# Kernel tuning notes

Measured on AMD Instinct MI355X. Metric: run time of the kernel, lower is better.

Reference implementation:

```python
import jax, jax.numpy as jnp
import numpy as np

B, T, D = 8, 4096, 256
GATE_MIN, GATE_MAX = 0.01, 0.99


def setup_inputs() -> dict:
    key = jax.random.key(0)
    ks = jax.random.split(key, 8)
    inp = {
        "x_re": jax.random.normal(ks[0], (B, T, D), jnp.float32),
        "x_im": jax.random.normal(ks[1], (B, T, D), jnp.float32),
        "s0_re": jnp.zeros((B, D), jnp.float32),
        "s0_im": jnp.zeros((B, D), jnp.float32),
        "decay_re": jax.random.normal(ks[2], (D,), jnp.float32),
        "decay_im": 0.1 * jax.random.normal(ks[3], (D,), jnp.float32),
        "Wm": 0.02 * jax.random.normal(ks[4], (2 * D, 2 * D), jnp.float32)
              + jnp.eye(2 * D, dtype=jnp.float32),  # eye_ init on diag blocks
        "bm": jnp.zeros((2 * D,), jnp.float32),
        "Wo": 0.02 * jax.random.normal(ks[5], (2 * D, 2 * D), jnp.float32),
        "bo": jnp.zeros((2 * D,), jnp.float32),
        "Wg": 0.02 * jax.random.normal(ks[6], (D, 2 * D), jnp.float32),
        "bg": jnp.zeros((D,), jnp.float32),
    }
    return inp


def reference(x_re, x_im, s0_re, s0_im, decay_re, decay_im,
              Wm, bm, Wo, bo, Wg, bg):
    # decay = sigmoid(decay_re) + i*decay_im
    dr = jax.nn.sigmoid(decay_re)
    di = decay_im

    # scan over time: inputs as [T, B, D]
    xs = (jnp.swapaxes(x_re, 0, 1), jnp.swapaxes(x_im, 0, 1))

    def step(carry, xt):
        s_re, s_im = carry
        xr, xi = xt                                   # [B, D]
        x_cat = jnp.concatenate([xr, xi], axis=-1)    # [B, 2D]
        x_in = x_cat @ Wm.T + bm
        ur, ui = jnp.split(x_in, 2, axis=-1)
        # complex mul-add: new_state = prev_state * decay + update
        ns_re = s_re * dr - s_im * di + ur
        ns_im = s_re * di + s_im * dr + ui
        s_cat = jnp.concatenate([ns_re, ns_im], axis=-1)  # [B, 2D]
        source = s_cat @ Wo.T + bo                        # [B, 2D] (re|im)
        gate = jnp.clip(jax.nn.sigmoid(s_cat @ Wg.T + bg), GATE_MIN, GATE_MAX)
        y = jnp.concatenate([source, gate], axis=-1)      # [B, 3D]
        return (ns_re, ns_im), y

    _, ys = jax.lax.scan(step, (s0_re, s0_im), xs)        # [T, B, 3D]
    return jnp.swapaxes(ys, 0, 1)                          # [B, T, 3D] = [src_re|src_im|gate]
```

## Files before the change

### kernel.cpp

```cpp
#include <hip/hip_runtime.h>
#include <hip/hip_bf16.h>
#include <cstdint>
#include <cstddef>


typedef __bf16 bf16;
typedef __bf16 bf16x4 __attribute__((ext_vector_type(4)));
typedef __bf16 bf16x8 __attribute__((ext_vector_type(8)));
typedef float floatx4 __attribute__((ext_vector_type(4)));

#define NB 8
#define NT 4096
#define ND 256
#define BT (NB * NT)
#define TWOD 512
#define CHUNK 128
#define NCHUNK (NT / CHUNK)

static __device__ __forceinline__ float sigmoidf_(float x) {
  return 1.0f / (1.0f + __expf(-x));
}

static __device__ __forceinline__ void async_copy16(const void* g, void* l) {
  __builtin_amdgcn_global_load_lds(
      (__attribute__((address_space(1))) void*)g,
      (__attribute__((address_space(3))) void*)l, 16, 0, 0);
}

__global__ void k_prep(const float* __restrict__ xr,
                       const float* __restrict__ xi,
                       const float* __restrict__ Wm,
                       const float* __restrict__ Wo,
                       const float* __restrict__ Wg,
                       const float* __restrict__ bo,
                       const float* __restrict__ bg,
                       bf16* __restrict__ X,
                       bf16* __restrict__ Wm_b,
                       bf16* __restrict__ Wc_b,
                       float* __restrict__ bc) {
  const int bid = blockIdx.x;
  if (bid < 8192) {
    const int idx = (bid * 256 + threadIdx.x) * 4;
    const int row = idx >> 8;
    const int dd = idx & 255;
    const float4 vr = *(const float4*)(xr + idx);
    const float4 vi = *(const float4*)(xi + idx);
    bf16x4 br, bi;
    br[0] = (bf16)vr.x; br[1] = (bf16)vr.y; br[2] = (bf16)vr.z; br[3] = (bf16)vr.w;
    bi[0] = (bf16)vi.x; bi[1] = (bf16)vi.y; bi[2] = (bf16)vi.z; bi[3] = (bf16)vi.w;
    *(bf16x4*)(X + (size_t)row * TWOD + dd) = br;
    *(bf16x4*)(X + (size_t)row * TWOD + ND + dd) = bi;
  } else {
    const int i = (bid - 8192) * 256 + threadIdx.x;
    Wm_b[i] = (bf16)Wm[i];
    Wc_b[i] = (bf16)Wo[i];
    if (i < 131072) Wc_b[262144 + i] = (bf16)Wg[i];
    if (i < 512) bc[i] = bo[i];
    if (i < 256) bc[512 + i] = bg[i];
  }
}

template <int MODE>
__global__ __launch_bounds__(256) void gemm_bt(
    const bf16* __restrict__ A, const bf16* __restrict__ Bw,
    const float* __restrict__ bias, void* __restrict__ Cout,
    const int K, const int N, const int actStart) {
  __shared__ __align__(16) bf16 As[128 * 64];
  __shared__ __align__(16) bf16 Bs[128 * 64];
  const int tid = threadIdx.x;
  const int wave = tid >> 6;
  const int lane = tid & 63;
  const int quad = lane >> 4;
  const int l16 = lane & 15;
  const int m0 = blockIdx.x * 128;
  const int n0 = blockIdx.y * 128;
  const int wm = (wave >> 1) * 64;
  const int wn = (wave & 1) * 64;

  const int srow = lane >> 3;
  const int schunk = (lane & 7) ^ (srow & 7);

  floatx4 acc[4][4];
#pragma unroll
  for (int i = 0; i < 4; ++i)
#pragma unroll
    for (int j = 0; j < 4; ++j) acc[i][j] = (floatx4)0.0f;

  for (int k0 = 0; k0 < K; k0 += 64) {
    __syncthreads();
#pragma unroll
    for (int i = 0; i < 4; ++i) {
      const int seg = wave * 4 + i;
      const int row = seg * 8 + srow;
      async_copy16(A + (size_t)(m0 + row) * K + k0 + schunk * 8, As + seg * 512);
      async_copy16(Bw + (size_t)(n0 + row) * K + k0 + schunk * 8, Bs + seg * 512);
    }
    __syncthreads();

#pragma unroll
    for (int s = 0; s < 2; ++s) {
      bf16x8 af[4], bfr[4];
#pragma unroll
      for (int mi = 0; mi < 4; ++mi) {
        const int row = wm + mi * 16 + l16;
        const int ch = ((s << 2) | quad) ^ (l16 & 7);
        af[mi] = *(const bf16x8*)(As + row * 64 + ch * 8);
      }
#pragma unroll
      for (int ni = 0; ni < 4; ++ni) {
        const int row = wn + ni * 16 + l16;
        const int ch = ((s << 2) | quad) ^ (l16 & 7);
        bfr[ni] = *(const bf16x8*)(Bs + row * 64 + ch * 8);
      }
#pragma unroll
      for (int mi = 0; mi < 4; ++mi)
#pragma unroll
        for (int ni = 0; ni < 4; ++ni)
          acc[mi][ni] = __builtin_amdgcn_mfma_f32_16x16x32_bf16(
              af[mi], bfr[ni], acc[mi][ni], 0, 0, 0);
    }
  }

#pragma unroll
  for (int mi = 0; mi < 4; ++mi) {
    const int rb = m0 + wm + mi * 16 + quad * 4;
#pragma unroll
    for (int ni = 0; ni < 4; ++ni) {
      const int col = n0 + wn + ni * 16 + l16;
      const float bb = bias[col];
      if (MODE == 0) {
        bf16* C = (bf16*)Cout;
#pragma unroll
        for (int r = 0; r < 4; ++r)
          C[(size_t)(rb + r) * N + col] = (bf16)(acc[mi][ni][r] + bb);
      } else {
        float* C = (float*)Cout;
#pragma unroll
        for (int r = 0; r < 4; ++r) {
          float v = acc[mi][ni][r] + bb;
          if (col >= actStart) v = fminf(fmaxf(sigmoidf_(v), 0.01f), 0.99f);
          C[(size_t)(rb + r) * N + col] = v;
        }
      }
    }
  }
}

__global__ void k_scan_pass1(const bf16* __restrict__ U,
                             const float* __restrict__ decay_re,
                             const float* __restrict__ decay_im,
                             float* __restrict__ Fre, float* __restrict__ Fim) {
  const int d = threadIdx.x;
  const int c = blockIdx.x;
  const int b = blockIdx.y;
  const float dr = sigmoidf_(decay_re[d]);
  const float di = decay_im[d];
  float sr = 0.f, si = 0.f;
  const size_t rowbase = (size_t)b * NT + (size_t)c * CHUNK;
  const bf16* Ur = U + rowbase * TWOD + d;
#pragma unroll 4
  for (int j = 0; j < CHUNK; ++j) {
    const float ur = (float)Ur[(size_t)j * TWOD];
    const float ui = (float)Ur[(size_t)j * TWOD + ND];
    const float nr = sr * dr - si * di + ur;
    const float ni = sr * di + si * dr + ui;
    sr = nr; si = ni;
  }
  const int o = (b * NCHUNK + c) * ND + d;
  Fre[o] = sr; Fim[o] = si;
}

__global__ void k_scan_pass2(const float* __restrict__ Fre,
                             const float* __restrict__ Fim,
                             const float* __restrict__ s0_re,
                             const float* __restrict__ s0_im,
                             const float* __restrict__ decay_re,
                             const float* __restrict__ decay_im,
                             float* __restrict__ Ire, float* __restrict__ Iim) {
  const int d = threadIdx.x;
  const int b = blockIdx.x;
  const float dr = sigmoidf_(decay_re[d]);
  const float di = decay_im[d];
  float pr = dr, pi = di;
#pragma unroll
  for (int i = 0; i < 7; ++i) {
    const float nr = pr * pr - pi * pi;
    const float ni = 2.f * pr * pi;
    pr = nr; pi = ni;
  }
  float sr = s0_re[b * ND + d];
  float si = s0_im[b * ND + d];
  for (int c = 0; c < NCHUNK; ++c) {
    const int o = (b * NCHUNK + c) * ND + d;
    Ire[o] = sr; Iim[o] = si;
    const float nr = sr * pr - si * pi + Fre[o];
    const float ni = sr * pi + si * pr + Fim[o];
    sr = nr; si = ni;
  }
}

__global__ void k_scan_pass3(bf16* __restrict__ U,
                             const float* __restrict__ decay_re,
                             const float* __restrict__ decay_im,
                             const float* __restrict__ Ire,
                             const float* __restrict__ Iim) {
  const int d = threadIdx.x;
  const int c = blockIdx.x;
  const int b = blockIdx.y;
  const float dr = sigmoidf_(decay_re[d]);
  const float di = decay_im[d];
  const int o = (b * NCHUNK + c) * ND + d;
  float sr = Ire[o], si = Iim[o];
  const size_t rowbase = (size_t)b * NT + (size_t)c * CHUNK;
  bf16* Ur = U + rowbase * TWOD + d;
#pragma unroll 4
  for (int j = 0; j < CHUNK; ++j) {
    const float ur = (float)Ur[(size_t)j * TWOD];
    const float ui = (float)Ur[(size_t)j * TWOD + ND];
    const float nr = sr * dr - si * di + ur;
    const float ni = sr * di + si * dr + ui;
    sr = nr; si = ni;
    Ur[(size_t)j * TWOD] = (bf16)nr;
    Ur[(size_t)j * TWOD + ND] = (bf16)ni;
  }
}


extern "C" void kernel_launch(void* const* d_in, const int* in_sizes, int n_in,
                              void* d_out, int out_size, void* d_ws, size_t ws_size,
                              hipStream_t stream) {
  const float* x_re = (const float*)d_in[0];
  const float* x_im = (const float*)d_in[1];
  const float* s0_re = (const float*)d_in[2];
  const float* s0_im = (const float*)d_in[3];
  const float* decay_re = (const float*)d_in[4];
  const float* decay_im = (const float*)d_in[5];
  const float* Wm = (const float*)d_in[6];
  const float* bm = (const float*)d_in[7];
  const float* Wo = (const float*)d_in[8];
  const float* bo = (const float*)d_in[9];
  const float* Wg = (const float*)d_in[10];
  const float* bg = (const float*)d_in[11];

  char* ws = (char*)d_ws;
  const size_t XCAT_OFF = 0;
  const size_t U_OFF = 33554432;
  const size_t WM_OFF = 67108864;
  const size_t WC_OFF = WM_OFF + 524288;
  const size_t BC_OFF = WC_OFF + 786432;
  const size_t FRE_OFF = BC_OFF + 4096;
  const size_t FIM_OFF = FRE_OFF + 262144;
  const size_t IRE_OFF = FIM_OFF + 262144;
  const size_t IIM_OFF = IRE_OFF + 262144;

  bf16* Xcat = (bf16*)(ws + XCAT_OFF);
  bf16* U = (bf16*)(ws + U_OFF);
  bf16* Wm_b = (bf16*)(ws + WM_OFF);
  bf16* Wc_b = (bf16*)(ws + WC_OFF);
  float* bc = (float*)(ws + BC_OFF);
  float* Fre = (float*)(ws + FRE_OFF);
  float* Fim = (float*)(ws + FIM_OFF);
  float* Ire = (float*)(ws + IRE_OFF);
  float* Iim = (float*)(ws + IIM_OFF);

  k_prep<<<dim3(9216), 256, 0, stream>>>(x_re, x_im, Wm, Wo, Wg, bo, bg,
                                         Xcat, Wm_b, Wc_b, bc);
  gemm_bt<0><<<dim3(256, 4), 256, 0, stream>>>(Xcat, Wm_b, bm, U, 512, 512, 0);
  k_scan_pass1<<<dim3(NCHUNK, NB), ND, 0, stream>>>(U, decay_re, decay_im, Fre, Fim);
  k_scan_pass2<<<dim3(NB), ND, 0, stream>>>(Fre, Fim, s0_re, s0_im, decay_re, decay_im, Ire, Iim);
  k_scan_pass3<<<dim3(NCHUNK, NB), ND, 0, stream>>>(U, decay_re, decay_im, Ire, Iim);
  gemm_bt<1><<<dim3(256, 6), 256, 0, stream>>>(U, Wc_b, bc, d_out, 512, 768, 512);
}
```

Measured before the change: 266.5 us.

## Fuse input bf16 conversion into GEMM, interleave re/im columns, shrink scan chunks

After: 259.8 us. -2.5%, faster.

```diff
diff --git a/kernel.cpp b/kernel.cpp
--- a/kernel.cpp
+++ b/kernel.cpp
@@ -5,7 +5,6 @@
 
 
 typedef __bf16 bf16;
-typedef __bf16 bf16x4 __attribute__((ext_vector_type(4)));
 typedef __bf16 bf16x8 __attribute__((ext_vector_type(8)));
 typedef float floatx4 __attribute__((ext_vector_type(4)));
 
@@ -14,7 +13,7 @@
 #define ND 256
 #define BT (NB * NT)
 #define TWOD 512
-#define CHUNK 128
+#define CHUNK 32
 #define NCHUNK (NT / CHUNK)
 
 static __device__ __forceinline__ float sigmoidf_(float x) {
@@ -27,44 +26,38 @@
       (__attribute__((address_space(3))) void*)l, 16, 0, 0);
 }
 
-__global__ void k_prep(const float* __restrict__ xr,
-                       const float* __restrict__ xi,
-                       const float* __restrict__ Wm,
+union U32BF2 { unsigned int u; __bf16 h[2]; };
+
+__global__ void k_prep(const float* __restrict__ Wm,
+                       const float* __restrict__ bm,
                        const float* __restrict__ Wo,
                        const float* __restrict__ Wg,
                        const float* __restrict__ bo,
                        const float* __restrict__ bg,
-                       bf16* __restrict__ X,
                        bf16* __restrict__ Wm_b,
                        bf16* __restrict__ Wc_b,
+                       float* __restrict__ bm_p,
                        float* __restrict__ bc) {
-  const int bid = blockIdx.x;
-  if (bid < 8192) {
-    const int idx = (bid * 256 + threadIdx.x) * 4;
-    const int row = idx >> 8;
-    const int dd = idx & 255;
-    const float4 vr = *(const float4*)(xr + idx);
-    const float4 vi = *(const float4*)(xi + idx);
-    bf16x4 br, bi;
-    br[0] = (bf16)vr.x; br[1] = (bf16)vr.y; br[2] = (bf16)vr.z; br[3] = (bf16)vr.w;
-    bi[0] = (bf16)vi.x; bi[1] = (bf16)vi.y; bi[2] = (bf16)vi.z; bi[3] = (bf16)vi.w;
-    *(bf16x4*)(X + (size_t)row * TWOD + dd) = br;
-    *(bf16x4*)(X + (size_t)row * TWOD + ND + dd) = bi;
-  } else {
-    const int i = (bid - 8192) * 256 + threadIdx.x;
-    Wm_b[i] = (bf16)Wm[i];
-    Wc_b[i] = (bf16)Wo[i];
-    if (i < 131072) Wc_b[262144 + i] = (bf16)Wg[i];
-    if (i < 512) bc[i] = bo[i];
-    if (i < 256) bc[512 + i] = bg[i];
-  }
-}
-
-template <int MODE>
-__global__ __launch_bounds__(256) void gemm_bt(
-    const bf16* __restrict__ A, const bf16* __restrict__ Bw,
-    const float* __restrict__ bias, void* __restrict__ Cout,
-    const int K, const int N, const int actStart) {
+  const int i = blockIdx.x * 256 + threadIdx.x;
+  {
+    const int r = i >> 9, c = i & 511;
+    const int sr = (r >> 1) + (r & 1) * 256;
+    Wm_b[i] = (bf16)Wm[sr * 512 + c];
+  }
+  {
+    const int r = i >> 9, c = i & 511;
+    const int sc = (c >> 1) + (c & 1) * 256;
+    Wc_b[i] = (bf16)Wo[r * 512 + sc];
+    if (i < 131072) Wc_b[262144 + i] = (bf16)Wg[r * 512 + sc];
+  }
+  if (i < 512) { bm_p[i] = bm[(i >> 1) + (i & 1) * 256]; bc[i] = bo[i]; }
+  if (i < 256) bc[512 + i] = bg[i];
+}
+
+__global__ __launch_bounds__(256) void gemm1(
+    const float* __restrict__ xre, const float* __restrict__ xim,
+    const bf16* __restrict__ Bw, const float* __restrict__ bias,
+    bf16* __restrict__ C) {
   __shared__ __align__(16) bf16 As[128 * 64];
   __shared__ __align__(16) bf16 Bs[128 * 64];
   const int tid = threadIdx.x;
@@ -76,9 +69,10 @@
   const int n0 = blockIdx.y * 128;
   const int wm = (wave >> 1) * 64;
   const int wn = (wave & 1) * 64;
-
   const int srow = lane >> 3;
   const int schunk = (lane & 7) ^ (srow & 7);
+  const int ar = tid >> 3;
+  const int sg = tid & 7;
 
   floatx4 acc[4][4];
 #pragma unroll
@@ -86,14 +80,27 @@
 #pragma unroll
     for (int j = 0; j < 4; ++j) acc[i][j] = (floatx4)0.0f;
 
-  for (int k0 = 0; k0 < K; k0 += 64) {
+  for (int k0 = 0; k0 < 512; k0 += 64) {
+    const float* xs = (k0 < 256) ? xre : xim;
+    const int xcol = k0 & 255;
     __syncthreads();
 #pragma unroll
     for (int i = 0; i < 4; ++i) {
       const int seg = wave * 4 + i;
       const int row = seg * 8 + srow;
-      async_copy16(A + (size_t)(m0 + row) * K + k0 + schunk * 8, As + seg * 512);
-      async_copy16(Bw + (size_t)(n0 + row) * K + k0 + schunk * 8, Bs + seg * 512);
+      async_copy16(Bw + (size_t)(n0 + row) * 512 + k0 + schunk * 8, Bs + seg * 512);
+    }
+#pragma unroll
+    for (int it = 0; it < 4; ++it) {
+      const int r = ar + 32 * it;
+      const int cg = sg ^ (r & 7);
+      const float* src = xs + (size_t)(m0 + r) * 256 + xcol + cg * 8;
+      const float4 f0 = *(const float4*)(src);
+      const float4 f1 = *(const float4*)(src + 4);
+      bf16x8 v;
+      v[0] = (bf16)f0.x; v[1] = (bf16)f0.y; v[2] = (bf16)f0.z; v[3] = (bf16)f0.w;
+      v[4] = (bf16)f1.x; v[5] = (bf16)f1.y; v[6] = (bf16)f1.z; v[7] = (bf16)f1.w;
+      *(bf16x8*)(As + r * 64 + sg * 8) = v;
     }
     __syncthreads();
 
@@ -128,19 +135,88 @@
     for (int ni = 0; ni < 4; ++ni) {
       const int col = n0 + wn + ni * 16 + l16;
       const float bb = bias[col];
-      if (MODE == 0) {
-        bf16* C = (bf16*)Cout;
-#pragma unroll
-        for (int r = 0; r < 4; ++r)
-          C[(size_t)(rb + r) * N + col] = (bf16)(acc[mi][ni][r] + bb);
-      } else {
-        float* C = (float*)Cout;
-#pragma unroll
-        for (int r = 0; r < 4; ++r) {
-          float v = acc[mi][ni][r] + bb;
-          if (col >= actStart) v = fminf(fmaxf(sigmoidf_(v), 0.01f), 0.99f);
-          C[(size_t)(rb + r) * N + col] = v;
-        }
+#pragma unroll
+      for (int r = 0; r < 4; ++r)
+        C[(size_t)(rb + r) * TWOD + col] = (bf16)(acc[mi][ni][r] + bb);
+    }
+  }
+}
+
+__global__ __launch_bounds__(256) void gemm2(
+    const bf16* __restrict__ A, const bf16* __restrict__ Bw,
+    const float* __restrict__ bias, float* __restrict__ C) {
+  __shared__ __align__(16) bf16 As[128 * 64];
+  __shared__ __align__(16) bf16 Bs[64 * 64];
+  const int tid = threadIdx.x;
+  const int wave = tid >> 6;
+  const int lane = tid & 63;
+  const int quad = lane >> 4;
+  const int l16 = lane & 15;
+  const int m0 = blockIdx.x * 128;
+  const int n0 = blockIdx.y * 64;
+  const int wm = (wave >> 1) * 64;
+  const int wn = (wave & 1) * 32;
+  const int srow = lane >> 3;
+  const int schunk = (lane & 7) ^ (srow & 7);
+
+  floatx4 acc[4][2];
+#pragma unroll
+  for (int i = 0; i < 4; ++i)
+#pragma unroll
+    for (int j = 0; j < 2; ++j) acc[i][j] = (floatx4)0.0f;
+
+  for (int k0 = 0; k0 < 512; k0 += 64) {
+    __syncthreads();
+#pragma unroll
+    for (int i = 0; i < 4; ++i) {
+      const int seg = wave * 4 + i;
+      const int row = seg * 8 + srow;
+      async_copy16(A + (size_t)(m0 + row) * 512 + k0 + schunk * 8, As + seg * 512);
+    }
+#pragma unroll
+    for (int i = 0; i < 2; ++i) {
+      const int seg = wave * 2 + i;
+      const int row = seg * 8 + srow;
+      async_copy16(Bw + (size_t)(n0 + row) * 512 + k0 + schunk * 8, Bs + seg * 512);
+    }
+    __syncthreads();
+
+#pragma unroll
+    for (int s = 0; s < 2; ++s) {
+      bf16x8 af[4], bfr[2];
+#pragma unroll
+      for (int mi = 0; mi < 4; ++mi) {
+        const int row = wm + mi * 16 + l16;
+        const int ch = ((s << 2) | quad) ^ (l16 & 7);
+        af[mi] = *(const bf16x8*)(As + row * 64 + ch * 8);
+      }
+#pragma unroll
+      for (int ni = 0; ni < 2; ++ni) {
+        const int row = wn + ni * 16 + l16;
+        const int ch = ((s << 2) | quad) ^ (l16 & 7);
+        bfr[ni] = *(const bf16x8*)(Bs + row * 64 + ch * 8);
+      }
+#pragma unroll
+      for (int mi = 0; mi < 4; ++mi)
+#pragma unroll
+        for (int ni = 0; ni < 2; ++ni)
+          acc[mi][ni] = __builtin_amdgcn_mfma_f32_16x16x32_bf16(
+              af[mi], bfr[ni], acc[mi][ni], 0, 0, 0);
+    }
+  }
+
+#pragma unroll
+  for (int mi = 0; mi < 4; ++mi) {
+    const int rb = m0 + wm + mi * 16 + quad * 4;
+#pragma unroll
+    for (int ni = 0; ni < 2; ++ni) {
+      const int col = n0 + wn + ni * 16 + l16;
+      const float bb = bias[col];
+#pragma unroll
+      for (int r = 0; r < 4; ++r) {
+        float v = acc[mi][ni][r] + bb;
+        if (col >= 512) v = fminf(fmaxf(sigmoidf_(v), 0.01f), 0.99f);
+        C[(size_t)(rb + r) * 768 + col] = v;
       }
     }
   }
@@ -156,12 +232,13 @@
   const float dr = sigmoidf_(decay_re[d]);
   const float di = decay_im[d];
   float sr = 0.f, si = 0.f;
-  const size_t rowbase = (size_t)b * NT + (size_t)c * CHUNK;
-  const bf16* Ur = U + rowbase * TWOD + d;
+  const unsigned int* Ur = (const unsigned int*)
+      (U + ((size_t)b * NT + (size_t)c * CHUNK) * TWOD + 2 * d);
 #pragma unroll 4
   for (int j = 0; j < CHUNK; ++j) {
-    const float ur = (float)Ur[(size_t)j * TWOD];
-    const float ui = (float)Ur[(size_t)j * TWOD + ND];
+    U32BF2 cv; cv.u = Ur[(size_t)j * (TWOD / 2)];
+    const float ur = (float)cv.h[0];
+    const float ui = (float)cv.h[1];
     const float nr = sr * dr - si * di + ur;
     const float ni = sr * di + si * dr + ui;
     sr = nr; si = ni;
@@ -183,7 +260,7 @@
   const float di = decay_im[d];
   float pr = dr, pi = di;
 #pragma unroll
-  for (int i = 0; i < 7; ++i) {
+  for (int i = 0; i < 5; ++i) {
     const float nr = pr * pr - pi * pi;
     const float ni = 2.f * pr * pi;
     pr = nr; pi = ni;
@@ -211,17 +288,18 @@
   const float di = decay_im[d];
   const int o = (b * NCHUNK + c) * ND + d;
   float sr = Ire[o], si = Iim[o];
-  const size_t rowbase = (size_t)b * NT + (size_t)c * CHUNK;
-  bf16* Ur = U + rowbase * TWOD + d;
+  unsigned int* Ur = (unsigned int*)
+      (U + ((size_t)b * NT + (size_t)c * CHUNK) * TWOD + 2 * d);
 #pragma unroll 4
   for (int j = 0; j < CHUNK; ++j) {
-    const float ur = (float)Ur[(size_t)j * TWOD];
-    const float ui = (float)Ur[(size_t)j * TWOD + ND];
+    U32BF2 cv; cv.u = Ur[(size_t)j * (TWOD / 2)];
+    const float ur = (float)cv.h[0];
+    const float ui = (float)cv.h[1];
     const float nr = sr * dr - si * di + ur;
     const float ni = sr * di + si * dr + ui;
     sr = nr; si = ni;
-    Ur[(size_t)j * TWOD] = (bf16)nr;
-    Ur[(size_t)j * TWOD + ND] = (bf16)ni;
+    cv.h[0] = (bf16)nr; cv.h[1] = (bf16)ni;
+    Ur[(size_t)j * (TWOD / 2)] = cv.u;
   }
 }
 
@@ -243,31 +321,32 @@
   const float* bg = (const float*)d_in[11];
 
   char* ws = (char*)d_ws;
-  const size_t XCAT_OFF = 0;
-  const size_t U_OFF = 33554432;
-  const size_t WM_OFF = 67108864;
+  const size_t U_OFF = 0;
+  const size_t WM_OFF = 33554432;
   const size_t WC_OFF = WM_OFF + 524288;
-  const size_t BC_OFF = WC_OFF + 786432;
+  const size_t BMP_OFF = WC_OFF + 786432;
+  const size_t BC_OFF = BMP_OFF + 4096;
   const size_t FRE_OFF = BC_OFF + 4096;
-  const size_t FIM_OFF = FRE_OFF + 262144;
-  const size_t IRE_OFF = FIM_OFF + 262144;
-  const size_t IIM_OFF = IRE_OFF + 262144;
-
-  bf16* Xcat = (bf16*)(ws + XCAT_OFF);
+  const size_t FIM_OFF = FRE_OFF + 1048576;
+  const size_t IRE_OFF = FIM_OFF + 1048576;
+  const size_t IIM_OFF = IRE_OFF + 1048576;
+
   bf16* U = (bf16*)(ws + U_OFF);
   bf16* Wm_b = (bf16*)(ws + WM_OFF);
   bf16* Wc_b = (bf16*)(ws + WC_OFF);
+  float* bm_p = (float*)(ws + BMP_OFF);
   float* bc = (float*)(ws + BC_OFF);
   float* Fre = (float*)(ws + FRE_OFF);
   float* Fim = (float*)(ws + FIM_OFF);
   float* Ire = (float*)(ws + IRE_OFF);
   float* Iim = (float*)(ws + IIM_OFF);
 
-  k_prep<<<dim3(9216), 256, 0, stream>>>(x_re, x_im, Wm, Wo, Wg, bo, bg,
-                                         Xcat, Wm_b, Wc_b, bc);
-  gemm_bt<0><<<dim3(256, 4), 256, 0, stream>>>(Xcat, Wm_b, bm, U, 512, 512, 0);
+  k_prep<<<dim3(1024), 256, 0, stream>>>(Wm, bm, Wo, Wg, bo, bg,
+                                         Wm_b, Wc_b, bm_p, bc);
+  gemm1<<<dim3(256, 4), 256, 0, stream>>>(x_re, x_im, Wm_b, bm_p, U);
   k_scan_pass1<<<dim3(NCHUNK, NB), ND, 0, stream>>>(U, decay_re, decay_im, Fre, Fim);
-  k_scan_pass2<<<dim3(NB), ND, 0, stream>>>(Fre, Fim, s0_re, s0_im, decay_re, decay_im, Ire, Iim);
+  k_scan_pass2<<<dim3(NB), ND, 0, stream>>>(Fre, Fim, s0_re, s0_im,
+                                            decay_re, decay_im, Ire, Iim);
   k_scan_pass3<<<dim3(NCHUNK, NB), ND, 0, stream>>>(U, decay_re, decay_im, Ire, Iim);
-  gemm_bt<1><<<dim3(256, 6), 256, 0, stream>>>(U, Wc_b, bc, d_out, 512, 768, 512);
-}
+  gemm2<<<dim3(256, 12), 256, 0, stream>>>(U, Wc_b, bc, (float*)d_out);
+}
```
